# Kernel optimization log

Measured on AMD Instinct MI355X. Metric: run time of the kernel, lower is better.

## Reference

```python
import jax, jax.numpy as jnp
import numpy as np

H = 300  # hidden size hardcoded in the module
VX = 32000
VY = 32000
NX, NY, B = 128, 128, 256


def setup_inputs() -> dict:
    key = jax.random.key(0)
    ks = jax.random.split(key, 10)
    s = 1.0 / np.sqrt(H)
    x = jax.random.randint(ks[0], (NX, B), 0, VX)
    y = jax.random.randint(ks[1], (NY, B), 0, VY)
    # padding_idx=0: zero the pad row of each embedding table
    enc_emb = jax.random.normal(ks[2], (VX, H), jnp.float32).at[0].set(0.0)
    encW = jax.random.uniform(ks[3], (H, H), jnp.float32, -s, s)
    encb = jax.random.uniform(ks[4], (H,), jnp.float32, -s, s)
    dec_emb = jax.random.normal(ks[5], (VY, H), jnp.float32).at[0].set(0.0)
    decW = jax.random.uniform(ks[6], (H, H), jnp.float32, -s, s)
    decb = jax.random.uniform(ks[7], (H,), jnp.float32, -s, s)
    outW = jax.random.uniform(ks[8], (VY, H), jnp.float32, -s, s)
    outb = jax.random.uniform(ks[9], (VY,), jnp.float32, -s, s)
    return {"x": x, "y": y, "enc_emb": enc_emb, "encW": encW, "encb": encb,
            "dec_emb": dec_emb, "decW": decW, "decb": decb,
            "outW": outW, "outb": outb}


def reference(x, y, enc_emb, encW, encb, dec_emb, decW, decb, outW, outb):
    # Encoder: Elman recurrence h = relu(e_x[i] + W h + b)
    e_x = enc_emb[x]                                  # [NX, B, H]
    h0 = jnp.zeros((x.shape[1], H), e_x.dtype)        # h=0 broadcast over batch

    def enc_step(h, ex):
        return jax.nn.relu(ex + h @ encW.T + encb), None

    h, _ = jax.lax.scan(enc_step, h0, e_x)

    # Decoder: teacher-forced recurrence with per-step mean cross-entropy
    e_y = dec_emb[y]                                  # [NY, B, H]

    def dec_step(h, inp):
        ey, tgt = inp
        h = jax.nn.relu(ey + h @ decW.T + decb)
        logits = h @ outW.T + outb                    # [B, VY]
        logp = jax.nn.log_softmax(logits, axis=-1)
        ce = -jnp.mean(jnp.take_along_axis(logp, tgt[:, None], axis=-1))
        return h, ce

    _, ces = jax.lax.scan(dec_step, h, (e_y[:-1], y[1:]))
    return jnp.sum(ces)
```

## Files before the change

### kernel.cpp

```cpp
#include <hip/hip_runtime.h>
#include <hip/hip_bf16.h>
#include <stdint.h>

typedef unsigned short u16;
typedef unsigned char u8;
typedef float f32x4 __attribute__((ext_vector_type(4)));
typedef float f32x2 __attribute__((ext_vector_type(2)));
typedef _Float16 f16x2 __attribute__((ext_vector_type(2)));
typedef _Float16 f16x8 __attribute__((ext_vector_type(8)));

#define H      300
#define KP     320
#define BATCH  256
#define NX     128
#define NY     128
#define VY     32000
#define NPAD   32768
#define MROWS  32512


#define OWS_OFF  0UL
#define OWS_BYTES ((unsigned long)NPAD * KP)
#define A8_OFF   (OWS_OFF + OWS_BYTES)
#define A8_BYTES ((unsigned long)MROWS * KP)
#define WTE_OFF  (A8_OFF + A8_BYTES)
#define WT_BYTES ((unsigned long)H * KP * 4)
#define WTD_OFF  (WTE_OFF + WT_BYTES)
#define SE_OFF   (WTD_OFF + WT_BYTES)
#define SE_BYTES ((unsigned long)MROWS * 4)

__global__ __launch_bounds__(256) void k0_prep(const float* __restrict__ outW,
                                               const float* __restrict__ encW,
                                               const float* __restrict__ decW,
                                               u8* __restrict__ ows,
                                               float* __restrict__ wte,
                                               float* __restrict__ wtd) {
    long id = (long)blockIdx.x * 256 + threadIdx.x;
    const long n1 = (long)NPAD * KP / 4;
    if (id < n1) {
        int v = (int)(id / 80), k4 = (int)(id % 80) * 4;
        float4 f = {0.f, 0.f, 0.f, 0.f};
        if (v < VY && k4 < H) f = *(const float4*)&outW[(long)v * H + k4];
        int w = __builtin_amdgcn_cvt_pk_fp8_f32(f.x, f.y, 0, false);
        w = __builtin_amdgcn_cvt_pk_fp8_f32(f.z, f.w, w, true);
        long dst = (long)(v >> 6) * 20480 + (k4 >> 5) * 2048 + ((v >> 4) & 3) * 512
                 + (v & 15) * 8 + ((k4 >> 3) & 3) * 128 + (k4 & 7);
        *(unsigned int*)(ows + dst) = (unsigned int)w;
        return;
    }
    long id2 = id - n1;
    if (id2 < (long)H * KP) {
        int k = (int)(id2 / KP), j = (int)(id2 % KP);
        wte[id2] = (j < H) ? encW[j * H + k] : 0.f;
        return;
    }
    id2 -= (long)H * KP;
    if (id2 < (long)H * KP) {
        int k = (int)(id2 / KP), j = (int)(id2 % KP);
        wtd[id2] = (j < H) ? decW[j * H + k] : 0.f;
    }
}

__global__ __launch_bounds__(960, 4) void k1_rnn(const int* __restrict__ x,
                                                 const int* __restrict__ y,
                                                 const float* __restrict__ enc_emb,
                                                 const float* __restrict__ dec_emb,
                                                 const float* __restrict__ encb,
                                                 const float* __restrict__ decb,
                                                 const float* __restrict__ wte,
                                                 const float* __restrict__ wtd,
                                                 u8* __restrict__ A8) {
    const int tid = threadIdx.x;
    const int s = tid / 320;
    const int j = tid - s * 320;
    const int b = blockIdx.x;

    __shared__ __align__(16) _Float16 hh[320];
    __shared__ float part[960];
    __shared__ __align__(4) u8 a8row[320];

    for (int i = tid; i < 320; i += 960) hh[i] = (_Float16)0.f;

    const bool comb = (tid < 320);
    const float be = (comb && j < H) ? encb[j] : 0.f;
    const float bd = (comb && j < H) ? decb[j] : 0.f;

    f16x2 w[52];
#pragma unroll
    for (int kk = 0; kk < 52; ++kk) {
        int k0 = 2 * (s * 52 + kk);
        float f0 = (k0 < H)     ? wte[k0 * KP + j]       : 0.f;
        float f1 = (k0 + 1 < H) ? wte[(k0 + 1) * KP + j] : 0.f;
        w[kk] = (f16x2){(_Float16)f0, (_Float16)f1};
    }

    int idx_n = x[BATCH + b];
    float e_cur = 0.f;
    if (comb && j < H) e_cur = enc_emb[(long)x[b] * H + j];
    __syncthreads();

    const f16x8* hb8 = (const f16x8*)&hh[s * 104];

    for (int t = 0; t < NX; ++t) {
        int idx_n2 = x[min(t + 2, NX - 1) * BATCH + b];
        float e_nx = 0.f;
        if (comb && j < H && t + 1 < NX) e_nx = enc_emb[(long)idx_n * H + j];

        float p0 = 0.f, p1 = 0.f;
#pragma unroll
        for (int i = 0; i < 13; ++i) {
            f16x8 hv = hb8[i];
            f16x2 a0 = {hv[0], hv[1]}, a1 = {hv[2], hv[3]};
            f16x2 a2 = {hv[4], hv[5]}, a3 = {hv[6], hv[7]};
            p0 = __builtin_amdgcn_fdot2(w[4 * i + 0], a0, p0, false);
            p1 = __builtin_amdgcn_fdot2(w[4 * i + 1], a1, p1, false);
            p0 = __builtin_amdgcn_fdot2(w[4 * i + 2], a2, p0, false);
            p1 = __builtin_amdgcn_fdot2(w[4 * i + 3], a3, p1, false);
        }
        part[tid] = p0 + p1;
        __syncthreads();
        if (comb) {
            float v = part[j] + part[320 + j] + part[640 + j] + be + e_cur;
            hh[j] = (_Float16)fmaxf(v, 0.f);
        }
        __syncthreads();
        e_cur = e_nx; idx_n = idx_n2;
    }

#pragma unroll
    for (int kk = 0; kk < 52; ++kk) {
        int k0 = 2 * (s * 52 + kk);
        float f0 = (k0 < H)     ? wtd[k0 * KP + j]       : 0.f;
        float f1 = (k0 + 1 < H) ? wtd[(k0 + 1) * KP + j] : 0.f;
        w[kk] = (f16x2){(_Float16)f0, (_Float16)f1};
    }

    idx_n = y[BATCH + b];
    e_cur = 0.f;
    if (comb && j < H) e_cur = dec_emb[(long)y[b] * H + j];

    for (int t = 0; t < NY - 1; ++t) {
        int idx_n2 = y[min(t + 2, NY - 1) * BATCH + b];
        float e_nx = 0.f;
        if (comb && j < H && t + 1 < NY - 1) e_nx = dec_emb[(long)idx_n * H + j];

        float p0 = 0.f, p1 = 0.f;
#pragma unroll
        for (int i = 0; i < 13; ++i) {
            f16x8 hv = hb8[i];
            f16x2 a0 = {hv[0], hv[1]}, a1 = {hv[2], hv[3]};
            f16x2 a2 = {hv[4], hv[5]}, a3 = {hv[6], hv[7]};
            p0 = __builtin_amdgcn_fdot2(w[4 * i + 0], a0, p0, false);
            p1 = __builtin_amdgcn_fdot2(w[4 * i + 1], a1, p1, false);
            p0 = __builtin_amdgcn_fdot2(w[4 * i + 2], a2, p0, false);
            p1 = __builtin_amdgcn_fdot2(w[4 * i + 3], a3, p1, false);
        }
        part[tid] = p0 + p1;
        __syncthreads();
        if (comb) {
            float v = part[j] + part[320 + j] + part[640 + j] + bd + e_cur;
            v = fmaxf(v, 0.f);
            hh[j] = (_Float16)v;
            int pk = __builtin_amdgcn_cvt_pk_fp8_f32(v, v, 0, false);
            a8row[j] = (u8)(pk & 0xff);
        }
        __syncthreads();
        if (tid < 80)
            ((unsigned int*)(A8 + (long)(t * BATCH + b) * KP))[tid] =
                ((const unsigned int*)a8row)[tid];
        e_cur = e_nx; idx_n = idx_n2;
    }
}

__global__ __launch_bounds__(256, 2) void k2_gemm(const u8* __restrict__ A8,
                                                  const u8* __restrict__ OWS,
                                                  const float* __restrict__ outb,
                                                  float* __restrict__ sumexp) {
    const int tid = threadIdx.x;
    const int lane = tid & 63, wave = tid >> 6;
    const int lane16 = lane & 15, quad = lane >> 4;
    const int cg = blockIdx.x & 7;
    const int rb = blockIdx.x >> 3;
    const int colbase = cg * 4096;

    __shared__ float rowsum[64];
    if (tid < 64) rowsum[tid] = 0.f;
    __syncthreads();

    long a[4][10];
    {
        const u8* abase = A8 + ((long)rb * 64 + lane16) * KP + quad * 8;
#pragma unroll
        for (int rt = 0; rt < 4; ++rt)
#pragma unroll
            for (int ks = 0; ks < 10; ++ks)
                a[rt][ks] = *(const long*)(abase + rt * 16 * KP + ks * 32);
    }

    const u8* wb = OWS + (long)(cg * 64 + wave) * 20480 + lane * 8;

    float rsum[16];
#pragma unroll
    for (int i = 0; i < 16; ++i) rsum[i] = 0.f;

    for (int ct = 0; ct < 16; ++ct) {
        const u8* ctp = wb + (long)ct * 4 * 20480;
        f32x4 acc[4][4];
#pragma unroll
        for (int p = 0; p < 4; ++p)
#pragma unroll
            for (int q = 0; q < 4; ++q) acc[p][q] = (f32x4){0.f, 0.f, 0.f, 0.f};

#pragma unroll
        for (int ks = 0; ks < 10; ++ks) {
            const u8* p = ctp + ks * 2048;
            long bfr[4];
#pragma unroll
            for (int tc = 0; tc < 4; ++tc)
                bfr[tc] = *(const long*)(p + tc * 512);
#pragma unroll
            for (int rt = 0; rt < 4; ++rt)
#pragma unroll
                for (int tc = 0; tc < 4; ++tc)
                    acc[rt][tc] = __builtin_amdgcn_mfma_f32_16x16x32_fp8_fp8(
                        a[rt][ks], bfr[tc], acc[rt][tc], 0, 0, 0);
        }

        int cb = colbase + ct * 256 + wave * 64;
#pragma unroll
        for (int tc = 0; tc < 4; ++tc) {
            int v = cb + tc * 16 + lane16;
            bool valid = v < VY;
            float ob = valid ? outb[v] : 0.f;
#pragma unroll
            for (int rt = 0; rt < 4; ++rt)
#pragma unroll
                for (int i = 0; i < 4; ++i) {
                    float lg = acc[rt][tc][i] + ob;
                    if (valid) rsum[rt * 4 + i] += __expf(lg);
                }
        }
    }

#pragma unroll
    for (int m = 1; m < 16; m <<= 1)
#pragma unroll
        for (int i = 0; i < 16; ++i) rsum[i] += __shfl_xor(rsum[i], m, 64);
    if (lane16 == 0) {
#pragma unroll
        for (int rt = 0; rt < 4; ++rt)
#pragma unroll
            for (int i = 0; i < 4; ++i)
                atomicAdd(&rowsum[rt * 16 + quad * 4 + i], rsum[rt * 4 + i]);
    }
    __syncthreads();
    if (tid < 64) atomicAdd(&sumexp[(long)rb * 64 + tid], rowsum[tid]);
}

__global__ __launch_bounds__(256) void k3_ce(const u8* __restrict__ A8,
                                             const u8* __restrict__ OWS,
                                             const float* __restrict__ outb,
                                             const float* __restrict__ sumexp,
                                             const int* __restrict__ y,
                                             float* __restrict__ out) {
    const int wave = threadIdx.x >> 6, lane = threadIdx.x & 63;
    const int r = blockIdx.x * 4 + wave;
    const int t = r >> 8, b = r & 255;
    const int tgt = y[(t + 1) * BATCH + b];
    float s = 0.f;
    if (lane < 40) {
        unsigned long long av = *(const unsigned long long*)(A8 + (long)r * KP + lane * 8);
        long wdst = (long)(tgt >> 6) * 20480 + (lane >> 2) * 2048
                  + ((tgt >> 4) & 3) * 512 + (tgt & 15) * 8 + (lane & 3) * 128;
        unsigned long long wv = *(const unsigned long long*)(OWS + wdst);
        unsigned int a4 = (unsigned int)av, a4h = (unsigned int)(av >> 32);
        unsigned int w4 = (unsigned int)wv, w4h = (unsigned int)(wv >> 32);
        f32x2 al = __builtin_amdgcn_cvt_pk_f32_fp8(a4, false);
        f32x2 ah = __builtin_amdgcn_cvt_pk_f32_fp8(a4, true);
        f32x2 wl = __builtin_amdgcn_cvt_pk_f32_fp8(w4, false);
        f32x2 wh = __builtin_amdgcn_cvt_pk_f32_fp8(w4, true);
        s += al[0] * wl[0] + al[1] * wl[1] + ah[0] * wh[0] + ah[1] * wh[1];
        al = __builtin_amdgcn_cvt_pk_f32_fp8(a4h, false);
        ah = __builtin_amdgcn_cvt_pk_f32_fp8(a4h, true);
        wl = __builtin_amdgcn_cvt_pk_f32_fp8(w4h, false);
        wh = __builtin_amdgcn_cvt_pk_f32_fp8(w4h, true);
        s += al[0] * wl[0] + al[1] * wl[1] + ah[0] * wh[0] + ah[1] * wh[1];
    }
#pragma unroll
    for (int m = 1; m < 64; m <<= 1) s += __shfl_xor(s, m, 64);
    __shared__ float part[4];
    if (lane == 0) part[wave] = logf(sumexp[r]) - (s + outb[tgt]);
    __syncthreads();
    if (threadIdx.x == 0) {
        float tot = part[0] + part[1] + part[2] + part[3];
        atomicAdd(out, tot * (1.0f / 256.0f));
    }
}

extern "C" void kernel_launch(void* const* d_in, const int* in_sizes, int n_in,
                              void* d_out, int out_size, void* d_ws, size_t ws_size,
                              hipStream_t stream) {
    (void)in_sizes; (void)n_in; (void)out_size; (void)ws_size;
    const int*   x       = (const int*)d_in[0];
    const int*   y       = (const int*)d_in[1];
    const float* enc_emb = (const float*)d_in[2];
    const float* encW    = (const float*)d_in[3];
    const float* encb    = (const float*)d_in[4];
    const float* dec_emb = (const float*)d_in[5];
    const float* decW    = (const float*)d_in[6];
    const float* decb    = (const float*)d_in[7];
    const float* outW    = (const float*)d_in[8];
    const float* outb    = (const float*)d_in[9];

    char* ws = (char*)d_ws;
    u8* ows  = (u8*)(ws + OWS_OFF);
    u8* A8   = (u8*)(ws + A8_OFF);
    float* wte    = (float*)(ws + WTE_OFF);
    float* wtd    = (float*)(ws + WTD_OFF);
    float* sumexp = (float*)(ws + SE_OFF);

    hipMemsetAsync(sumexp, 0, SE_BYTES, stream);
    hipMemsetAsync(d_out, 0, sizeof(float), stream);

    long n0 = (long)NPAD * KP / 4 + 2L * H * KP;
    k0_prep<<<(int)((n0 + 255) / 256), 256, 0, stream>>>(outW, encW, decW, ows, wte, wtd);
    k1_rnn<<<256, 960, 0, stream>>>(x, y, enc_emb, dec_emb, encb, decb, wte, wtd, A8);
    k2_gemm<<<508 * 8, 256, 0, stream>>>(A8, ows, outb, sumexp);
    k3_ce<<<8128, 256, 0, stream>>>(A8, ows, outb, sumexp, y, (float*)d_out);
}
```

Baseline: 1.039 ms.

## Stage A in LDS, software-pipeline B loads in GEMM, reshape RNN threads

The logits GEMM now stages the 64-row fp8 activation tile in padded shared memory instead of holding it in registers. It prefetches B fragments two k-steps ahead in a rotating register buffer and flattens the column-tile loop so loads overlap the MFMAs, with occupancy raised to 3 blocks. The bias is pre-padded with -1e30 so invalid columns need no branch. The RNN kernel drops from 960 to 640 threads, each computing two output columns over an 80-wide K slice with four partial sums, trading register pressure and barrier overhead. Prefetching past the last tile reads into an added padding region of the workspace.

New measurement: 2.244 ms. 2.16x slower.

```diff
diff --git a/kernel.cpp b/kernel.cpp
--- a/kernel.cpp
+++ b/kernel.cpp
@@ -19,20 +19,25 @@
 #define MROWS  32512
 
 
-#define OWS_OFF  0UL
+#define OWS_OFF   0UL
 #define OWS_BYTES ((unsigned long)NPAD * KP)
-#define A8_OFF   (OWS_OFF + OWS_BYTES)
-#define A8_BYTES ((unsigned long)MROWS * KP)
-#define WTE_OFF  (A8_OFF + A8_BYTES)
-#define WT_BYTES ((unsigned long)H * KP * 4)
-#define WTD_OFF  (WTE_OFF + WT_BYTES)
-#define SE_OFF   (WTD_OFF + WT_BYTES)
-#define SE_BYTES ((unsigned long)MROWS * 4)
+#define OWS_PAD   131072UL
+#define A8_OFF    (OWS_OFF + OWS_BYTES + OWS_PAD)
+#define A8_BYTES  ((unsigned long)MROWS * KP)
+#define WTE_OFF   (A8_OFF + A8_BYTES)
+#define WT_BYTES  (320UL * KP * 4)
+#define WTD_OFF   (WTE_OFF + WT_BYTES)
+#define OBP_OFF   (WTD_OFF + WT_BYTES)
+#define OBP_BYTES ((unsigned long)NPAD * 4)
+#define SE_OFF    (OBP_OFF + OBP_BYTES)
+#define SE_BYTES  ((unsigned long)MROWS * 4)
 
 __global__ __launch_bounds__(256) void k0_prep(const float* __restrict__ outW,
                                                const float* __restrict__ encW,
                                                const float* __restrict__ decW,
+                                               const float* __restrict__ outb,
                                                u8* __restrict__ ows,
+                                               float* __restrict__ obp,
                                                float* __restrict__ wte,
                                                float* __restrict__ wtd) {
     long id = (long)blockIdx.x * 256 + threadIdx.x;
@@ -49,120 +54,134 @@
         return;
     }
     long id2 = id - n1;
-    if (id2 < (long)H * KP) {
+    if (id2 < NPAD) {
+        obp[id2] = (id2 < VY) ? outb[id2] : -1e30f;
+        return;
+    }
+    id2 -= NPAD;
+    if (id2 < 320L * KP) {
         int k = (int)(id2 / KP), j = (int)(id2 % KP);
-        wte[id2] = (j < H) ? encW[j * H + k] : 0.f;
+        wte[id2] = (k < H && j < H) ? encW[j * H + k] : 0.f;
         return;
     }
-    id2 -= (long)H * KP;
-    if (id2 < (long)H * KP) {
+    id2 -= 320L * KP;
+    if (id2 < 320L * KP) {
         int k = (int)(id2 / KP), j = (int)(id2 % KP);
-        wtd[id2] = (j < H) ? decW[j * H + k] : 0.f;
-    }
-}
-
-__global__ __launch_bounds__(960, 4) void k1_rnn(const int* __restrict__ x,
-                                                 const int* __restrict__ y,
-                                                 const float* __restrict__ enc_emb,
-                                                 const float* __restrict__ dec_emb,
-                                                 const float* __restrict__ encb,
-                                                 const float* __restrict__ decb,
-                                                 const float* __restrict__ wte,
-                                                 const float* __restrict__ wtd,
-                                                 u8* __restrict__ A8) {
+        wtd[id2] = (k < H && j < H) ? decW[j * H + k] : 0.f;
+    }
+}
+
+__global__ __launch_bounds__(640) void k1_rnn(const int* __restrict__ x,
+                                              const int* __restrict__ y,
+                                              const float* __restrict__ enc_emb,
+                                              const float* __restrict__ dec_emb,
+                                              const float* __restrict__ encb,
+                                              const float* __restrict__ decb,
+                                              const float* __restrict__ wte,
+                                              const float* __restrict__ wtd,
+                                              u8* __restrict__ A8) {
     const int tid = threadIdx.x;
-    const int s = tid / 320;
-    const int j = tid - s * 320;
+    const int s = tid / 160;
+    const int j = tid - s * 160;
     const int b = blockIdx.x;
 
     __shared__ __align__(16) _Float16 hh[320];
-    __shared__ float part[960];
+    __shared__ float part[1280];
     __shared__ __align__(4) u8 a8row[320];
 
-    for (int i = tid; i < 320; i += 960) hh[i] = (_Float16)0.f;
+    for (int i = tid; i < 320; i += 640) hh[i] = (_Float16)0.f;
 
     const bool comb = (tid < 320);
-    const float be = (comb && j < H) ? encb[j] : 0.f;
-    const float bd = (comb && j < H) ? decb[j] : 0.f;
-
-    f16x2 w[52];
-#pragma unroll
-    for (int kk = 0; kk < 52; ++kk) {
-        int k0 = 2 * (s * 52 + kk);
-        float f0 = (k0 < H)     ? wte[k0 * KP + j]       : 0.f;
-        float f1 = (k0 + 1 < H) ? wte[(k0 + 1) * KP + j] : 0.f;
-        w[kk] = (f16x2){(_Float16)f0, (_Float16)f1};
+    const int jc = tid;
+    const float be = (comb && jc < H) ? encb[jc] : 0.f;
+    const float bd = (comb && jc < H) ? decb[jc] : 0.f;
+
+    f16x2 wa[40], wc[40];
+#pragma unroll
+    for (int kk = 0; kk < 40; ++kk) {
+        int k0 = s * 80 + 2 * kk;
+        wa[kk] = (f16x2){(_Float16)wte[k0 * KP + j],       (_Float16)wte[(k0 + 1) * KP + j]};
+        wc[kk] = (f16x2){(_Float16)wte[k0 * KP + j + 160], (_Float16)wte[(k0 + 1) * KP + j + 160]};
     }
 
     int idx_n = x[BATCH + b];
     float e_cur = 0.f;
-    if (comb && j < H) e_cur = enc_emb[(long)x[b] * H + j];
+    if (comb && jc < H) e_cur = enc_emb[(long)x[b] * H + jc];
     __syncthreads();
 
-    const f16x8* hb8 = (const f16x8*)&hh[s * 104];
+    const f16x8* hb8 = (const f16x8*)&hh[s * 80];
 
     for (int t = 0; t < NX; ++t) {
         int idx_n2 = x[min(t + 2, NX - 1) * BATCH + b];
         float e_nx = 0.f;
-        if (comb && j < H && t + 1 < NX) e_nx = enc_emb[(long)idx_n * H + j];
+        if (comb && jc < H && t + 1 < NX) e_nx = enc_emb[(long)idx_n * H + jc];
 
         float p0 = 0.f, p1 = 0.f;
 #pragma unroll
-        for (int i = 0; i < 13; ++i) {
+        for (int i = 0; i < 10; ++i) {
             f16x8 hv = hb8[i];
-            f16x2 a0 = {hv[0], hv[1]}, a1 = {hv[2], hv[3]};
-            f16x2 a2 = {hv[4], hv[5]}, a3 = {hv[6], hv[7]};
-            p0 = __builtin_amdgcn_fdot2(w[4 * i + 0], a0, p0, false);
-            p1 = __builtin_amdgcn_fdot2(w[4 * i + 1], a1, p1, false);
-            p0 = __builtin_amdgcn_fdot2(w[4 * i + 2], a2, p0, false);
-            p1 = __builtin_amdgcn_fdot2(w[4 * i + 3], a3, p1, false);
-        }
-        part[tid] = p0 + p1;
+            f16x2 q0 = {hv[0], hv[1]}, q1 = {hv[2], hv[3]};
+            f16x2 q2 = {hv[4], hv[5]}, q3 = {hv[6], hv[7]};
+            p0 = __builtin_amdgcn_fdot2(wa[4 * i + 0], q0, p0, false);
+            p1 = __builtin_amdgcn_fdot2(wc[4 * i + 0], q0, p1, false);
+            p0 = __builtin_amdgcn_fdot2(wa[4 * i + 1], q1, p0, false);
+            p1 = __builtin_amdgcn_fdot2(wc[4 * i + 1], q1, p1, false);
+            p0 = __builtin_amdgcn_fdot2(wa[4 * i + 2], q2, p0, false);
+            p1 = __builtin_amdgcn_fdot2(wc[4 * i + 2], q2, p1, false);
+            p0 = __builtin_amdgcn_fdot2(wa[4 * i + 3], q3, p0, false);
+            p1 = __builtin_amdgcn_fdot2(wc[4 * i + 3], q3, p1, false);
+        }
+        part[s * 320 + j] = p0;
+        part[s * 320 + 160 + j] = p1;
         __syncthreads();
         if (comb) {
-            float v = part[j] + part[320 + j] + part[640 + j] + be + e_cur;
-            hh[j] = (_Float16)fmaxf(v, 0.f);
+            float v = part[jc] + part[320 + jc] + part[640 + jc] + part[960 + jc] + be + e_cur;
+            hh[jc] = (_Float16)fmaxf(v, 0.f);
         }
         __syncthreads();
         e_cur = e_nx; idx_n = idx_n2;
     }
 
 #pragma unroll
-    for (int kk = 0; kk < 52; ++kk) {
-        int k0 = 2 * (s * 52 + kk);
-        float f0 = (k0 < H)     ? wtd[k0 * KP + j]       : 0.f;
-        float f1 = (k0 + 1 < H) ? wtd[(k0 + 1) * KP + j] : 0.f;
-        w[kk] = (f16x2){(_Float16)f0, (_Float16)f1};
+    for (int kk = 0; kk < 40; ++kk) {
+        int k0 = s * 80 + 2 * kk;
+        wa[kk] = (f16x2){(_Float16)wtd[k0 * KP + j],       (_Float16)wtd[(k0 + 1) * KP + j]};
+        wc[kk] = (f16x2){(_Float16)wtd[k0 * KP + j + 160], (_Float16)wtd[(k0 + 1) * KP + j + 160]};
     }
 
     idx_n = y[BATCH + b];
     e_cur = 0.f;
-    if (comb && j < H) e_cur = dec_emb[(long)y[b] * H + j];
+    if (comb && jc < H) e_cur = dec_emb[(long)y[b] * H + jc];
 
     for (int t = 0; t < NY - 1; ++t) {
         int idx_n2 = y[min(t + 2, NY - 1) * BATCH + b];
         float e_nx = 0.f;
-        if (comb && j < H && t + 1 < NY - 1) e_nx = dec_emb[(long)idx_n * H + j];
+        if (comb && jc < H && t + 1 < NY - 1) e_nx = dec_emb[(long)idx_n * H + jc];
 
         float p0 = 0.f, p1 = 0.f;
 #pragma unroll
-        for (int i = 0; i < 13; ++i) {
+        for (int i = 0; i < 10; ++i) {
             f16x8 hv = hb8[i];
-            f16x2 a0 = {hv[0], hv[1]}, a1 = {hv[2], hv[3]};
-            f16x2 a2 = {hv[4], hv[5]}, a3 = {hv[6], hv[7]};
-            p0 = __builtin_amdgcn_fdot2(w[4 * i + 0], a0, p0, false);
-            p1 = __builtin_amdgcn_fdot2(w[4 * i + 1], a1, p1, false);
-            p0 = __builtin_amdgcn_fdot2(w[4 * i + 2], a2, p0, false);
-            p1 = __builtin_amdgcn_fdot2(w[4 * i + 3], a3, p1, false);
-        }
-        part[tid] = p0 + p1;
+            f16x2 q0 = {hv[0], hv[1]}, q1 = {hv[2], hv[3]};
+            f16x2 q2 = {hv[4], hv[5]}, q3 = {hv[6], hv[7]};
+            p0 = __builtin_amdgcn_fdot2(wa[4 * i + 0], q0, p0, false);
+            p1 = __builtin_amdgcn_fdot2(wc[4 * i + 0], q0, p1, false);
+            p0 = __builtin_amdgcn_fdot2(wa[4 * i + 1], q1, p0, false);
+            p1 = __builtin_amdgcn_fdot2(wc[4 * i + 1], q1, p1, false);
+            p0 = __builtin_amdgcn_fdot2(wa[4 * i + 2], q2, p0, false);
+            p1 = __builtin_amdgcn_fdot2(wc[4 * i + 2], q2, p1, false);
+            p0 = __builtin_amdgcn_fdot2(wa[4 * i + 3], q3, p0, false);
+            p1 = __builtin_amdgcn_fdot2(wc[4 * i + 3], q3, p1, false);
+        }
+        part[s * 320 + j] = p0;
+        part[s * 320 + 160 + j] = p1;
         __syncthreads();
         if (comb) {
-            float v = part[j] + part[320 + j] + part[640 + j] + bd + e_cur;
+            float v = part[jc] + part[320 + jc] + part[640 + jc] + part[960 + jc] + bd + e_cur;
             v = fmaxf(v, 0.f);
-            hh[j] = (_Float16)v;
+            hh[jc] = (_Float16)v;
             int pk = __builtin_amdgcn_cvt_pk_fp8_f32(v, v, 0, false);
-            a8row[j] = (u8)(pk & 0xff);
+            a8row[jc] = (u8)(pk & 0xff);
         }
         __syncthreads();
         if (tid < 80)
@@ -172,9 +191,9 @@
     }
 }
 
-__global__ __launch_bounds__(256, 2) void k2_gemm(const u8* __restrict__ A8,
+__global__ __launch_bounds__(256, 3) void k2_gemm(const u8* __restrict__ A8,
                                                   const u8* __restrict__ OWS,
-                                                  const float* __restrict__ outb,
+                                                  const float* __restrict__ obp,
                                                   float* __restrict__ sumexp) {
     const int tid = threadIdx.x;
     const int lane = tid & 63, wave = tid >> 6;
@@ -183,63 +202,80 @@
     const int rb = blockIdx.x >> 3;
     const int colbase = cg * 4096;
 
+    __shared__ u8 Ald[64 * 336];
     __shared__ float rowsum[64];
     if (tid < 64) rowsum[tid] = 0.f;
+
+    {
+        const u8* ag = A8 + (long)rb * 64 * KP;
+#pragma unroll
+        for (int i = 0; i < 5; ++i) {
+            int t2 = i * 256 + tid;
+            int row = t2 / 20, o = t2 % 20;
+            *(uint4*)&Ald[row * 336 + o * 16] = *(const uint4*)(ag + row * 320 + o * 16);
+        }
+    }
     __syncthreads();
 
-    long a[4][10];
-    {
-        const u8* abase = A8 + ((long)rb * 64 + lane16) * KP + quad * 8;
-#pragma unroll
-        for (int rt = 0; rt < 4; ++rt)
-#pragma unroll
-            for (int ks = 0; ks < 10; ++ks)
-                a[rt][ks] = *(const long*)(abase + rt * 16 * KP + ks * 32);
-    }
-
     const u8* wb = OWS + (long)(cg * 64 + wave) * 20480 + lane * 8;
 
+    long bb[4][4];
+#pragma unroll
+    for (int tc = 0; tc < 4; ++tc) {
+        bb[0][tc] = *(const long*)(wb + tc * 512);
+        bb[1][tc] = *(const long*)(wb + 2048 + tc * 512);
+    }
+
+    f32x4 acc[4][4];
+#pragma unroll
+    for (int p = 0; p < 4; ++p)
+#pragma unroll
+        for (int q = 0; q < 4; ++q) acc[p][q] = (f32x4){0.f, 0.f, 0.f, 0.f};
+
     float rsum[16];
 #pragma unroll
     for (int i = 0; i < 16; ++i) rsum[i] = 0.f;
 
-    for (int ct = 0; ct < 16; ++ct) {
-        const u8* ctp = wb + (long)ct * 4 * 20480;
-        f32x4 acc[4][4];
-#pragma unroll
-        for (int p = 0; p < 4; ++p)
-#pragma unroll
-            for (int q = 0; q < 4; ++q) acc[p][q] = (f32x4){0.f, 0.f, 0.f, 0.f};
-
-#pragma unroll
-        for (int ks = 0; ks < 10; ++ks) {
-            const u8* p = ctp + ks * 2048;
-            long bfr[4];
-#pragma unroll
-            for (int tc = 0; tc < 4; ++tc)
-                bfr[tc] = *(const long*)(p + tc * 512);
+    const u8* pB = wb;
+    for (int cc = 0; cc < 8; ++cc) {
+#pragma unroll
+        for (int u = 0; u < 20; ++u) {
+            const int ks = (u < 10) ? u : u - 10;
+            {
+                const int u2 = u + 2;
+                const u8* pf = pB + (u2 / 10) * 81920 + (u2 % 10) * 2048;
+#pragma unroll
+                for (int tc = 0; tc < 4; ++tc)
+                    bb[(u + 2) & 3][tc] = *(const long*)(pf + tc * 512);
+            }
+            long av[4];
+#pragma unroll
+            for (int rt = 0; rt < 4; ++rt)
+                av[rt] = *(const long*)&Ald[(rt * 16 + lane16) * 336 + ks * 32 + quad * 8];
 #pragma unroll
             for (int rt = 0; rt < 4; ++rt)
 #pragma unroll
                 for (int tc = 0; tc < 4; ++tc)
                     acc[rt][tc] = __builtin_amdgcn_mfma_f32_16x16x32_fp8_fp8(
-                        a[rt][ks], bfr[tc], acc[rt][tc], 0, 0, 0);
-        }
-
-        int cb = colbase + ct * 256 + wave * 64;
-#pragma unroll
-        for (int tc = 0; tc < 4; ++tc) {
-            int v = cb + tc * 16 + lane16;
-            bool valid = v < VY;
-            float ob = valid ? outb[v] : 0.f;
-#pragma unroll
-            for (int rt = 0; rt < 4; ++rt)
-#pragma unroll
-                for (int i = 0; i < 4; ++i) {
-                    float lg = acc[rt][tc][i] + ob;
-                    if (valid) rsum[rt * 4 + i] += __expf(lg);
+                        av[rt], bb[u & 3][tc], acc[rt][tc], 0, 0, 0);
+
+            if (ks == 9) {
+                int ct = cc * 2 + (u >= 10);
+                int cb = colbase + ct * 256 + wave * 64;
+#pragma unroll
+                for (int tc = 0; tc < 4; ++tc) {
+                    float ob = obp[cb + tc * 16 + lane16];
+#pragma unroll
+                    for (int rt = 0; rt < 4; ++rt) {
+#pragma unroll
+                        for (int i = 0; i < 4; ++i)
+                            rsum[rt * 4 + i] += __expf(acc[rt][tc][i] + ob);
+                        acc[rt][tc] = (f32x4){0.f, 0.f, 0.f, 0.f};
+                    }
                 }
-        }
+            }
+        }
+        pB += 163840;
     }
 
 #pragma unroll
@@ -317,14 +353,16 @@
     u8* A8   = (u8*)(ws + A8_OFF);
     float* wte    = (float*)(ws + WTE_OFF);
     float* wtd    = (float*)(ws + WTD_OFF);
+    float* obp    = (float*)(ws + OBP_OFF);
     float* sumexp = (float*)(ws + SE_OFF);
 
     hipMemsetAsync(sumexp, 0, SE_BYTES, stream);
     hipMemsetAsync(d_out, 0, sizeof(float), stream);
 
-    long n0 = (long)NPAD * KP / 4 + 2L * H * KP;
-    k0_prep<<<(int)((n0 + 255) / 256), 256, 0, stream>>>(outW, encW, decW, ows, wte, wtd);
-    k1_rnn<<<256, 960, 0, stream>>>(x, y, enc_emb, dec_emb, encb, decb, wte, wtd, A8);
-    k2_gemm<<<508 * 8, 256, 0, stream>>>(A8, ows, outb, sumexp);
+    long n0 = (long)NPAD * KP / 4 + NPAD + 2L * 320 * KP;
+    k0_prep<<<(int)((n0 + 255) / 256), 256, 0, stream>>>(outW, encW, decW, outb,
+                                                         ows, obp, wte, wtd);
+    k1_rnn<<<256, 640, 0, stream>>>(x, y, enc_emb, dec_emb, encb, decb, wte, wtd, A8);
+    k2_gemm<<<508 * 8, 256, 0, stream>>>(A8, ows, obp, sumexp);
     k3_ce<<<8128, 256, 0, stream>>>(A8, ows, outb, sumexp, y, (float*)d_out);
 }
```
